# Kernel tuning notes

Hardware: AMD Instinct MI355X
Metric: run time of the kernel (lower is better)

## Reference

```python
import jax, jax.numpy as jnp
import numpy as np

SEQ = 512; WIN = [4, 4, 4]; INNER = 5; DM = 256; H = 4; DK = 64; NEG = -1e9

def _all_sizes():
    s = [SEQ]
    for w in WIN:
        s.append(s[-1] // w)
    return s

def _build_mask():
    # Pyraformer get_mask: intra-scale band (inner_size) + inter-scale parent/child links.
    sizes = _all_sizes(); N = sum(sizes)
    starts = np.cumsum([0] + sizes)
    allow = np.zeros((N, N), bool)
    iw = INNER // 2
    for li, sz in enumerate(sizes):
        st = int(starts[li])
        for i in range(st, st + sz):
            allow[i, max(i - iw, st):min(i + iw + 1, st + sz)] = True
    for li in range(1, len(sizes)):
        st = int(starts[li])
        for i in range(st, st + sizes[li]):
            ls = int(starts[li - 1]) + (i - st) * WIN[li - 1]
            rs = st if i == st + sizes[li] - 1 else int(starts[li - 1]) + (i - st + 1) * WIN[li - 1]
            allow[i, ls:rs] = True
            allow[ls:rs, i] = True
    return jnp.asarray(~allow)  # True = blocked

def _build_indexes():
    # Pyraformer refer_points: for each base position, index of its node at every scale.
    sizes = _all_sizes(); starts = np.cumsum([0] + sizes)
    idx = np.zeros((SEQ, len(sizes)), np.int32)
    for i in range(SEQ):
        cur = i
        idx[i, 0] = cur
        for j in range(1, len(sizes)):
            inner = cur - int(starts[j - 1])
            cur = int(starts[j]) + min(inner // WIN[j - 1], sizes[j] - 1)
            idx[i, j] = cur
    return jnp.asarray(idx)

def _pos_enc(L, D):
    pos = np.arange(L)[:, None]
    div = np.exp(np.arange(0, D, 2) * (-np.log(10000.0) / D))
    pe = np.zeros((L, D), np.float32)
    pe[:, 0::2] = np.sin(pos * div)
    pe[:, 1::2] = np.cos(pos * div)
    return jnp.asarray(pe)

MASK = _build_mask()
INDEXES = _build_indexes()
PE = _pos_enc(SEQ, DM)
DN = ('NCH', 'OIH', 'NCH')

def _ln(x, g, b, eps=1e-5):
    m = x.mean(-1, keepdims=True)
    v = ((x - m) ** 2).mean(-1, keepdims=True)
    return (x - m) * jax.lax.rsqrt(v + eps) * g + b

def _forward(x_enc, x_mark, W_val, W_time, b_time, W_down, b_down, W_conv, b_conv, bn_g, bn_b, W_up, b_up, ln_c_g, ln_c_b, Wq, bq, Wk, bk, Wv, bv, Wo, bo, ln1_g, ln1_b, W1f, b1f, W2f, b2f, ln2_g, ln2_b, Wp, bp):
    B = x_enc.shape[0]
    # DataEmbedding: circular k=3 token conv + time-feature linear + fixed positional
    xt = jnp.pad(x_enc.transpose(0, 2, 1), ((0, 0), (0, 0), (1, 1)), mode='wrap')
    val = jax.lax.conv_general_dilated(xt, W_val, (1,), 'VALID', dimension_numbers=DN).transpose(0, 2, 1)
    emb = val + x_mark @ W_time + b_time + PE[None]  # [B, SEQ, DM]
    # CSCM Bottleneck_Construct: down-proj, strided conv pooling per scale, up-proj, concat, LN
    t = (emb @ W_down + b_down).transpose(0, 2, 1)  # [B, 64, SEQ]
    pooled = []
    for i in range(len(WIN)):
        t = jax.lax.conv_general_dilated(t, W_conv[i], (WIN[i],), 'VALID', dimension_numbers=DN) + b_conv[i][None, :, None]
        t = jax.nn.elu(t * bn_g[i][None, :, None] + bn_b[i][None, :, None])
        pooled.append(t)
    pooled = jnp.concatenate(pooled, axis=2).transpose(0, 2, 1) @ W_up + b_up  # [B, 168, DM]
    x = _ln(jnp.concatenate([emb, pooled], axis=1), ln_c_g, ln_c_b)  # [B, 680, DM]
    N = x.shape[1]
    scale = np.float32(1.0 / np.sqrt(DK))
    for l in range(Wq.shape[0]):
        q = (x @ Wq[l] + bq[l]).reshape(B, N, H, DK).transpose(0, 2, 1, 3)
        k = (x @ Wk[l] + bk[l]).reshape(B, N, H, DK).transpose(0, 2, 1, 3)
        v = (x @ Wv[l] + bv[l]).reshape(B, N, H, DK).transpose(0, 2, 1, 3)
        s = jnp.einsum('bhqd,bhkd->bhqk', q, k) * scale
        s = jnp.where(MASK[None, None], NEG, s)
        o = jnp.einsum('bhqk,bhkd->bhqd', jax.nn.softmax(s, axis=-1), v)
        o = o.transpose(0, 2, 1, 3).reshape(B, N, DM) @ Wo[l] + bo[l]
        x = _ln(x + o, ln1_g[l], ln1_b[l])  # post-norm (normalize_before=False)
        f = jax.nn.relu(x @ W1f[l] + b1f[l]) @ W2f[l] + b2f[l]
        x = _ln(x + f, ln2_g[l], ln2_b[l])
    # FC decoder path: gather each position's multi-scale nodes, concat features
    gathered = x[:, INDEXES.reshape(-1)].reshape(B, SEQ, -1)  # [B, SEQ, 4*DM]
    return gathered[:, -1] @ Wp + bp  # [B, 96]

def setup_inputs() -> dict:
    key = jax.random.key(0)
    ks = iter(jax.random.split(key, 64))
    def w(shape, s=0.05):
        return jax.random.normal(next(ks), shape, jnp.float32) * s
    d = {}
    d['x_enc'] = jax.random.normal(next(ks), (32, SEQ, 1), jnp.float32)
    d['x_mark'] = jax.random.normal(next(ks), (32, SEQ, 4), jnp.float32)
    d['W_val'] = w((DM, 1, 3))
    d['W_time'] = w((4, DM)); d['b_time'] = jnp.zeros((DM,), jnp.float32)
    d['W_down'] = w((DM, 64)); d['b_down'] = jnp.zeros((64,), jnp.float32)
    d['W_conv'] = w((3, 64, 64, 4)); d['b_conv'] = jnp.zeros((3, 64), jnp.float32)
    d['bn_g'] = jnp.ones((3, 64), jnp.float32); d['bn_b'] = jnp.zeros((3, 64), jnp.float32)
    d['W_up'] = w((64, DM)); d['b_up'] = jnp.zeros((DM,), jnp.float32)
    d['ln_c_g'] = jnp.ones((DM,), jnp.float32); d['ln_c_b'] = jnp.zeros((DM,), jnp.float32)
    d['Wq'] = w((2, DM, DM)); d['bq'] = jnp.zeros((2, DM), jnp.float32)
    d['Wk'] = w((2, DM, DM)); d['bk'] = jnp.zeros((2, DM), jnp.float32)
    d['Wv'] = w((2, DM, DM)); d['bv'] = jnp.zeros((2, DM), jnp.float32)
    d['Wo'] = w((2, DM, DM)); d['bo'] = jnp.zeros((2, DM), jnp.float32)
    d['ln1_g'] = jnp.ones((2, DM), jnp.float32); d['ln1_b'] = jnp.zeros((2, DM), jnp.float32)
    d['W1f'] = w((2, DM, 512)); d['b1f'] = jnp.zeros((2, 512), jnp.float32)
    d['W2f'] = w((2, 512, DM)); d['b2f'] = jnp.zeros((2, DM), jnp.float32)
    d['ln2_g'] = jnp.ones((2, DM), jnp.float32); d['ln2_b'] = jnp.zeros((2, DM), jnp.float32)
    d['Wp'] = w((4 * DM, 96)); d['bp'] = jnp.zeros((96,), jnp.float32)
    return d

def reference(x_enc, x_mark, W_val, W_time, b_time, W_down, b_down, W_conv, b_conv, bn_g, bn_b, W_up, b_up, ln_c_g, ln_c_b, Wq, bq, Wk, bk, Wv, bv, Wo, bo, ln1_g, ln1_b, W1f, b1f, W2f, b2f, ln2_g, ln2_b, Wp, bp):
    return _forward(x_enc, x_mark, W_val, W_time, b_time, W_down, b_down, W_conv, b_conv, bn_g, bn_b, W_up, b_up, ln_c_g, ln_c_b, Wq, bq, Wk, bk, Wv, bv, Wo, bo, ln1_g, ln1_b, W1f, b1f, W2f, b2f, ln2_g, ln2_b, Wp, bp)
```

## Files before the change

kernel.cpp:

```cpp
#include <hip/hip_runtime.h>
#include <hip/hip_bf16.h>
#include <math.h>

#define B 32
#define SEQ 512
#define NTOK 680
#define DM 256
#define FF 512
#define NROWS (B*NTOK)

using bf16x8 = __attribute__((ext_vector_type(8))) short;
using f32x4  = __attribute__((ext_vector_type(4))) float;
using u32x4  = __attribute__((ext_vector_type(4))) unsigned int;
typedef __hip_bfloat16 bf16;

__device__ __forceinline__ unsigned short f2bf(float f) {
    union { float f; unsigned u; } x; x.f = f;
    unsigned r = (x.u + 0x7fffu + ((x.u >> 16) & 1u)) >> 16;
    return (unsigned short)r;
}
__device__ __forceinline__ float bfu2f(unsigned short u) {
    union { unsigned u; float f; } x; x.u = ((unsigned)u) << 16;
    return x.f;
}
__device__ __forceinline__ void dotu(unsigned a, unsigned b, float& s) {
    union { unsigned u; float f; } al, ah, bl, bh;
    al.u = a << 16; ah.u = a & 0xffff0000u;
    bl.u = b << 16; bh.u = b & 0xffff0000u;
    s = fmaf(al.f, bl.f, s);
    s = fmaf(ah.f, bh.f, s);
}

__global__ __launch_bounds__(256) void emb_kernel(
    const float* __restrict__ x_enc, const float* __restrict__ x_mark,
    const float* __restrict__ W_val, const float* __restrict__ W_time,
    const float* __restrict__ b_time, float* __restrict__ X, bf16* __restrict__ Xe)
{
    int bs = blockIdx.x;
    int b = bs >> 9, s = bs & 511;
    int d = threadIdx.x;
    int sm1 = (s + 511) & 511, sp1 = (s + 1) & 511;
    float x0 = x_enc[b*512 + sm1];
    float x1 = x_enc[b*512 + s];
    float x2 = x_enc[b*512 + sp1];
    float val = x0 * W_val[d*3+0] + x1 * W_val[d*3+1] + x2 * W_val[d*3+2];
    const float* mk = &x_mark[(size_t)bs*4];
    float tm = mk[0]*W_time[d] + mk[1]*W_time[256+d] + mk[2]*W_time[512+d] + mk[3]*W_time[768+d];
    int i2 = d & ~1;
    float div = expf((float)i2 * (-9.210340371976184f / 256.0f));
    float ang = (float)s * div;
    float pe = (d & 1) ? cosf(ang) : sinf(ang);
    float out = val + tm + b_time[d] + pe;
    X[((size_t)(b*NTOK + s))*DM + d] = out;
    ((unsigned short*)Xe)[(size_t)bs*DM + d] = f2bf(out);
}

__global__ __launch_bounds__(64) void conv_kernel(
    const float* __restrict__ in, int inRPB, int inOff,
    float* __restrict__ Pool, int outOff, int Lout,
    const float* __restrict__ W_conv, const float* __restrict__ b_conv,
    const float* __restrict__ bn_g, const float* __restrict__ bn_b, int sc)
{
    __shared__ float lds[256];
    int blk = blockIdx.x;
    int b = blk / Lout, p = blk % Lout;
    int t = threadIdx.x;
    for (int u = t; u < 256; u += 64)
        lds[u] = in[((size_t)(b*inRPB + inOff + p*4 + (u >> 6)))*64 + (u & 63)];
    __syncthreads();
    float acc = b_conv[sc*64 + t];
    const float* w = &W_conv[(size_t)(sc*64 + t)*256];
    #pragma unroll 4
    for (int ci = 0; ci < 64; ++ci) {
        #pragma unroll
        for (int tap = 0; tap < 4; ++tap)
            acc = fmaf(lds[tap*64 + ci], w[ci*4 + tap], acc);
    }
    float v = acc * bn_g[sc*64 + t] + bn_b[sc*64 + t];
    v = v > 0.f ? v : expm1f(v);
    Pool[((size_t)(b*168 + outOff + p))*64 + t] = v;
}

__global__ __launch_bounds__(256) void up_kernel(
    const float* __restrict__ Pool, const float* __restrict__ W_up,
    const float* __restrict__ b_up, float* __restrict__ X)
{
    __shared__ float row[64];
    int blk = blockIdx.x;
    int b = blk / 168, p = blk % 168;
    int d = threadIdx.x;
    if (d < 64) row[d] = Pool[(size_t)blk*64 + d];
    __syncthreads();
    float acc = b_up[d];
    #pragma unroll 8
    for (int k = 0; k < 64; ++k) acc = fmaf(row[k], W_up[k*256 + d], acc);
    X[((size_t)(b*NTOK + 512 + p))*DM + d] = acc;
}

__global__ __launch_bounds__(256) void ln_kernel(
    const float* __restrict__ Xf, bf16* __restrict__ Xio,
    const float* __restrict__ g, const float* __restrict__ bta)
{
    int r = blockIdx.x*4 + (threadIdx.x >> 6);
    int lane = threadIdx.x & 63;
    float4 v = ((const float4*)(Xf + (size_t)r*DM))[lane];
    float s = v.x + v.y + v.z + v.w;
    #pragma unroll
    for (int o = 32; o; o >>= 1) s += __shfl_xor(s, o);
    float mean = s * (1.0f/256.0f);
    float dx = v.x-mean, dy = v.y-mean, dz = v.z-mean, dw = v.w-mean;
    float q = dx*dx + dy*dy + dz*dz + dw*dw;
    #pragma unroll
    for (int o = 32; o; o >>= 1) q += __shfl_xor(q, o);
    float inv = rsqrtf(q*(1.0f/256.0f) + 1e-5f);
    float4 gg = ((const float4*)g)[lane];
    float4 bb = ((const float4*)bta)[lane];
    float ox = dx*inv*gg.x + bb.x;
    float oy = dy*inv*gg.y + bb.y;
    float oz = dz*inv*gg.z + bb.z;
    float ow = dw*inv*gg.w + bb.w;
    unsigned u0 = (unsigned)f2bf(ox) | ((unsigned)f2bf(oy) << 16);
    unsigned u1 = (unsigned)f2bf(oz) | ((unsigned)f2bf(ow) << 16);
    ((uint2*)(Xio + (size_t)r*DM))[lane] = make_uint2(u0, u1);
}

__global__ void nbr_kernel(int* __restrict__ nbr, int* __restrict__ ncnt)
{
    int i = blockIdx.x * 64 + threadIdx.x;
    if (i >= NTOK) return;
    const int starts[5] = {0, 512, 640, 672, 680};
    int si = (i < 512) ? 0 : (i < 640) ? 1 : (i < 672) ? 2 : 3;
    int st = starts[si], en = starts[si+1];
    int idx = i - st;
    int cnt = 0;
    if (si >= 1) {
        int cs = starts[si-1] + idx*4;
        #pragma unroll
        for (int c = 0; c < 4; ++c) nbr[i*16 + cnt++] = cs + c;
    }
    int lo = (i-2 > st) ? i-2 : st;
    int hi = (i+2 < en-1) ? i+2 : en-1;
    for (int j = lo; j <= hi; ++j) nbr[i*16 + cnt++] = j;
    if (si <= 2) nbr[i*16 + cnt++] = starts[si+1] + (idx >> 2);
    ncnt[i] = cnt;
}

__global__ __launch_bounds__(256) void attn_kernel(
    const bf16* __restrict__ Q, const bf16* __restrict__ K,
    const bf16* __restrict__ V, bf16* __restrict__ O,
    const int* __restrict__ nbr, const int* __restrict__ ncnt)
{
    __shared__ float wsm[4][16];
    __shared__ int   jsm[4][16];
    int flat = blockIdx.x;
    int row = (flat & 7) * (NROWS/8) + (flat >> 3);
    int n = row % NTOK, b = row / NTOK;
    int h = threadIdx.x >> 6;
    int lane = threadIdx.x & 63;
    int j = lane >> 2, g = lane & 3;
    int cnt = ncnt[n];
    int nj = (j < cnt) ? nbr[n*16 + j] : n;
    int jr = b*NTOK + nj;

    const uint4* qp = (const uint4*)(Q + (size_t)row*DM + h*64 + g*16);
    const uint4* kp = (const uint4*)(K + (size_t)jr*DM + h*64 + g*16);
    uint4 qa = qp[0], qb = qp[1];
    uint4 ka = kp[0], kb = kp[1];
    float s = 0.f;
    dotu(qa.x, ka.x, s); dotu(qa.y, ka.y, s); dotu(qa.z, ka.z, s); dotu(qa.w, ka.w, s);
    dotu(qb.x, kb.x, s); dotu(qb.y, kb.y, s); dotu(qb.z, kb.z, s); dotu(qb.w, kb.w, s);
    s += __shfl_xor(s, 1);
    s += __shfl_xor(s, 2);
    s *= 0.125f;
    if (j >= cnt) s = -1e30f;
    float m = s;
    #pragma unroll
    for (int o = 4; o < 64; o <<= 1) m = fmaxf(m, __shfl_xor(m, o));
    float w = (j < cnt) ? expf(s - m) : 0.f;
    float den = w;
    #pragma unroll
    for (int o = 4; o < 64; o <<= 1) den += __shfl_xor(den, o);
    if (g == 0) { wsm[h][j] = w / den; jsm[h][j] = jr; }
    __syncthreads();

    float acc = 0.f;
    const unsigned short* Vu = (const unsigned short*)V;
    for (int jj = 0; jj < cnt; ++jj) {
        float wv = wsm[h][jj];
        int rr = jsm[h][jj];
        acc = fmaf(wv, bfu2f(Vu[(size_t)rr*DM + h*64 + lane]), acc);
    }
    ((unsigned short*)O)[(size_t)row*DM + h*64 + lane] = f2bf(acc);
}

struct WDesc { const float* src; bf16* dst; int K; int N; };
struct WTable { WDesc d[13]; };
__global__ __launch_bounds__(256) void wconv_kernel(WTable tbl)
{
    __shared__ float lds[32][33];
    WDesc ds = tbl.d[blockIdx.y];
    int ntn = ds.N >> 5;
    int ntiles = (ds.K >> 5) * ntn;
    int tile = blockIdx.x;
    if (tile >= ntiles) return;
    int k0 = (tile / ntn) * 32, n0 = (tile % ntn) * 32;
    int t = threadIdx.x;
    int r = t >> 3, c4 = (t & 7) * 4;
    float4 v = *(const float4*)(ds.src + (size_t)(k0 + r)*ds.N + n0 + c4);
    lds[r][c4+0] = v.x; lds[r][c4+1] = v.y; lds[r][c4+2] = v.z; lds[r][c4+3] = v.w;
    __syncthreads();
    unsigned u0 = (unsigned)f2bf(lds[c4+0][r]) | ((unsigned)f2bf(lds[c4+1][r]) << 16);
    unsigned u1 = (unsigned)f2bf(lds[c4+2][r]) | ((unsigned)f2bf(lds[c4+3][r]) << 16);
    *(uint2*)((unsigned short*)ds.dst + (size_t)(n0 + r)*ds.K + k0 + c4) = make_uint2(u0, u1);
}

#define CSTR 260
__global__ __launch_bounds__(512) void wo_ln_kernel(
    const bf16* __restrict__ Ob, bf16* __restrict__ Xh,
    const bf16* __restrict__ WoT, const float* __restrict__ bo,
    const float* __restrict__ g, const float* __restrict__ bta)
{
    __shared__ __align__(16) char smem[16384 + 33280];
    uint4* AsU = (uint4*)smem;
    const bf16x8* Asv = (const bf16x8*)smem;
    float* ctile = (float*)(smem + 16384);

    int t = threadIdx.x;
    int lane = t & 63, w = t >> 6;
    int nwg = gridDim.x;
    int wg = (blockIdx.x & 7) * (nwg >> 3) + (blockIdx.x >> 3);
    int row0 = wg * 32;
    const unsigned short* Obu = (const unsigned short*)Ob;
    const unsigned short* Xu  = (const unsigned short*)Xh;
    const unsigned short* Wu  = (const unsigned short*)WoT;

    #pragma unroll
    for (int i = 0; i < 2; ++i) {
        int gg = t + i*512, r = gg >> 5, c = gg & 31;
        AsU[r*32 + (c ^ (r & 7))] = *(const uint4*)(Obu + (size_t)(row0 + r)*DM + c*8);
    }

    f32x4 acc[2][2];
    #pragma unroll
    for (int m = 0; m < 2; ++m)
        #pragma unroll
        for (int nn = 0; nn < 2; ++nn)
            #pragma unroll
            for (int q = 0; q < 4; ++q) acc[m][nn][q] = 0.f;
    float bv[2];
    #pragma unroll
    for (int nn = 0; nn < 2; ++nn) bv[nn] = bo[w*32 + nn*16 + (lane & 15)];
    __syncthreads();

    #pragma unroll
    for (int kt = 0; kt < 256; kt += 32) {
        int cg = (kt >> 3) + (lane >> 4);
        bf16x8 af[2];
        #pragma unroll
        for (int m = 0; m < 2; ++m) {
            int ar = m*16 + (lane & 15);
            af[m] = Asv[ar*32 + (cg ^ (ar & 7))];
        }
        #pragma unroll
        for (int nn = 0; nn < 2; ++nn) {
            int nrow = w*32 + nn*16 + (lane & 15);
            bf16x8 bfr = *(const bf16x8*)(Wu + (size_t)nrow*256 + kt + (lane >> 4)*8);
            #pragma unroll
            for (int m = 0; m < 2; ++m)
                acc[m][nn] = __builtin_amdgcn_mfma_f32_16x16x32_bf16(af[m], bfr, acc[m][nn], 0, 0, 0);
        }
    }

    __syncthreads();
    #pragma unroll
    for (int m = 0; m < 2; ++m)
        #pragma unroll
        for (int nn = 0; nn < 2; ++nn) {
            int col = w*32 + nn*16 + (lane & 15);
            #pragma unroll
            for (int q = 0; q < 4; ++q) {
                int row = m*16 + (lane >> 4)*4 + q;
                ctile[row*CSTR + col] = acc[m][nn][q] + bv[nn];
            }
        }
    __syncthreads();
    #pragma unroll
    for (int rr = 0; rr < 4; ++rr) {
        int row = w*4 + rr;
        float4 v = *(const float4*)(ctile + row*CSTR + lane*4);
        uint2 xu = *(const uint2*)(Xu + (size_t)(row0 + row)*DM + lane*4);
        v.x += bfu2f((unsigned short)(xu.x & 0xffffu));
        v.y += bfu2f((unsigned short)(xu.x >> 16));
        v.z += bfu2f((unsigned short)(xu.y & 0xffffu));
        v.w += bfu2f((unsigned short)(xu.y >> 16));
        float s = v.x + v.y + v.z + v.w;
        #pragma unroll
        for (int o = 32; o; o >>= 1) s += __shfl_xor(s, o);
        float mean = s * (1.0f/256.0f);
        float dx = v.x-mean, dy = v.y-mean, dz = v.z-mean, dw = v.w-mean;
        float q2 = dx*dx + dy*dy + dz*dz + dw*dw;
        #pragma unroll
        for (int o = 32; o; o >>= 1) q2 += __shfl_xor(q2, o);
        float inv = rsqrtf(q2*(1.0f/256.0f) + 1e-5f);
        float4 gg = ((const float4*)g)[lane];
        float4 bb = ((const float4*)bta)[lane];
        float ox = dx*inv*gg.x + bb.x;
        float oy = dy*inv*gg.y + bb.y;
        float oz = dz*inv*gg.z + bb.z;
        float ow = dw*inv*gg.w + bb.w;
        unsigned u0 = (unsigned)f2bf(ox) | ((unsigned)f2bf(oy) << 16);
        unsigned u1 = (unsigned)f2bf(oz) | ((unsigned)f2bf(ow) << 16);
        *(uint2*)((unsigned short*)Xh + (size_t)(row0 + row)*DM + lane*4) = make_uint2(u0, u1);
    }
}

#define HSTR 280
__global__ __launch_bounds__(512) void ff_kernel(
    bf16* __restrict__ Xh,
    const bf16* __restrict__ W1t, const float* __restrict__ b1,
    const bf16* __restrict__ W2t, const float* __restrict__ b2,
    const float* __restrict__ g, const float* __restrict__ bta)
{
    __shared__ __align__(16) char smem[16384 + 33280];
    uint4* AsU = (uint4*)smem;
    const bf16x8* Asv = (const bf16x8*)smem;
    unsigned short* hT = (unsigned short*)(smem + 16384);
    float* ctile = (float*)(smem + 16384);

    int t = threadIdx.x;
    int lane = t & 63, w = t >> 6;
    int nwg = gridDim.x;
    int wg = (blockIdx.x & 7) * (nwg >> 3) + (blockIdx.x >> 3);
    int row0 = wg * 32;
    const unsigned short* Xu = (const unsigned short*)Xh;

    #pragma unroll
    for (int i = 0; i < 2; ++i) {
        int gg = t + i*512, r = gg >> 5, c = gg & 31;
        AsU[r*32 + (c ^ (r & 7))] = *(const uint4*)(Xu + (size_t)(row0 + r)*DM + c*8);
    }

    f32x4 acc2[2][2];
    #pragma unroll
    for (int m = 0; m < 2; ++m)
        #pragma unroll
        for (int nn = 0; nn < 2; ++nn)
            #pragma unroll
            for (int q = 0; q < 4; ++q) acc2[m][nn][q] = 0.f;
    float b2v[2];
    #pragma unroll
    for (int nn = 0; nn < 2; ++nn) b2v[nn] = b2[w*32 + nn*16 + (lane & 15)];
    __syncthreads();

    const unsigned short* W1u = (const unsigned short*)W1t;
    const unsigned short* W2u = (const unsigned short*)W2t;

    #pragma unroll
    for (int half = 0; half < 2; ++half) {
        f32x4 acc1[2][2];
        #pragma unroll
        for (int m = 0; m < 2; ++m)
            #pragma unroll
            for (int nn = 0; nn < 2; ++nn)
                #pragma unroll
                for (int q = 0; q < 4; ++q) acc1[m][nn][q] = 0.f;
        #pragma unroll
        for (int kt = 0; kt < 256; kt += 32) {
            int cg = (kt >> 3) + (lane >> 4);
            bf16x8 af[2];
            #pragma unroll
            for (int m = 0; m < 2; ++m) {
                int ar = m*16 + (lane & 15);
                af[m] = Asv[ar*32 + (cg ^ (ar & 7))];
            }
            #pragma unroll
            for (int nn = 0; nn < 2; ++nn) {
                int nrow = half*256 + w*32 + nn*16 + (lane & 15);
                bf16x8 bfr = *(const bf16x8*)(W1u + (size_t)nrow*256 + kt + (lane >> 4)*8);
                #pragma unroll
                for (int m = 0; m < 2; ++m)
                    acc1[m][nn] = __builtin_amdgcn_mfma_f32_16x16x32_bf16(af[m], bfr, acc1[m][nn], 0, 0, 0);
            }
        }
        float b1v[2];
        #pragma unroll
        for (int nn = 0; nn < 2; ++nn) b1v[nn] = b1[half*256 + w*32 + nn*16 + (lane & 15)];
        __syncthreads();
        #pragma unroll
        for (int m = 0; m < 2; ++m)
            #pragma unroll
            for (int nn = 0; nn < 2; ++nn) {
                int col = w*32 + nn*16 + (lane & 15);
                #pragma unroll
                for (int q = 0; q < 4; ++q) {
                    int row = m*16 + (lane >> 4)*4 + q;
                    hT[row*HSTR + col] = f2bf(fmaxf(acc1[m][nn][q] + b1v[nn], 0.f));
                }
            }
        __syncthreads();
        #pragma unroll
        for (int kt = 0; kt < 256; kt += 32) {
            bf16x8 af[2];
            #pragma unroll
            for (int m = 0; m < 2; ++m) {
                int ar = m*16 + (lane & 15);
                af[m] = *(const bf16x8*)(hT + ar*HSTR + kt + (lane >> 4)*8);
            }
            #pragma unroll
            for (int nn = 0; nn < 2; ++nn) {
                int nrow = w*32 + nn*16 + (lane & 15);
                bf16x8 bfr = *(const bf16x8*)(W2u + (size_t)nrow*512 + half*256 + kt + (lane >> 4)*8);
                #pragma unroll
                for (int m = 0; m < 2; ++m)
                    acc2[m][nn] = __builtin_amdgcn_mfma_f32_16x16x32_bf16(af[m], bfr, acc2[m][nn], 0, 0, 0);
            }
        }
    }
    __syncthreads();
    #pragma unroll
    for (int m = 0; m < 2; ++m)
        #pragma unroll
        for (int nn = 0; nn < 2; ++nn) {
            int col = w*32 + nn*16 + (lane & 15);
            #pragma unroll
            for (int q = 0; q < 4; ++q) {
                int row = m*16 + (lane >> 4)*4 + q;
                ctile[row*CSTR + col] = acc2[m][nn][q] + b2v[nn];
            }
        }
    __syncthreads();
    #pragma unroll
    for (int rr = 0; rr < 4; ++rr) {
        int row = w*4 + rr;
        float4 v = *(const float4*)(ctile + row*CSTR + lane*4);
        uint2 xu = *(const uint2*)(Xu + (size_t)(row0 + row)*DM + lane*4);
        v.x += bfu2f((unsigned short)(xu.x & 0xffffu));
        v.y += bfu2f((unsigned short)(xu.x >> 16));
        v.z += bfu2f((unsigned short)(xu.y & 0xffffu));
        v.w += bfu2f((unsigned short)(xu.y >> 16));
        float s = v.x + v.y + v.z + v.w;
        #pragma unroll
        for (int o = 32; o; o >>= 1) s += __shfl_xor(s, o);
        float mean = s * (1.0f/256.0f);
        float dx = v.x-mean, dy = v.y-mean, dz = v.z-mean, dw = v.w-mean;
        float q2 = dx*dx + dy*dy + dz*dz + dw*dw;
        #pragma unroll
        for (int o = 32; o; o >>= 1) q2 += __shfl_xor(q2, o);
        float inv = rsqrtf(q2*(1.0f/256.0f) + 1e-5f);
        float4 gg = ((const float4*)g)[lane];
        float4 bb = ((const float4*)bta)[lane];
        float ox = dx*inv*gg.x + bb.x;
        float oy = dy*inv*gg.y + bb.y;
        float oz = dz*inv*gg.z + bb.z;
        float ow = dw*inv*gg.w + bb.w;
        unsigned u0 = (unsigned)f2bf(ox) | ((unsigned)f2bf(oy) << 16);
        unsigned u1 = (unsigned)f2bf(oz) | ((unsigned)f2bf(ow) << 16);
        *(uint2*)((unsigned short*)Xh + (size_t)(row0 + row)*DM + lane*4) = make_uint2(u0, u1);
    }
}

template<int KD, int NY, int NZ, bool RELU>
__global__ __launch_bounds__(256) void mfma_gemm_fr(
    const bf16* __restrict__ A,
    const bf16* __restrict__ Wt0, const bf16* __restrict__ Wt1, const bf16* __restrict__ Wt2,
    const float* __restrict__ b0, const float* __restrict__ b1, const float* __restrict__ b2,
    bf16* __restrict__ O0, bf16* __restrict__ O1, bf16* __restrict__ O2,
    int Nc, int totalWg)
{
    __shared__ __align__(16) char smem[24576];
    uint4* AsU = (uint4*)smem;
    uint4* BsU = (uint4*)(smem + 8192);
    const bf16x8* Asv = (const bf16x8*)smem;
    const bf16x8* Bsv = (const bf16x8*)(smem + 8192);

    int t = threadIdx.x;
    int lane = t & 63, wid = t >> 6;
    int nwg = gridDim.x;
    int wg = (blockIdx.x & 7) * (nwg >> 3) + (blockIdx.x >> 3);
    if (wg >= totalWg) return;
    int xt = wg / (NY*NZ);
    int rem = wg % (NY*NZ);
    int z = rem / NY;
    int y = rem % NY;
    int row0 = xt * 64;
    int n0 = y * 128;
    const bf16* W = ((z == 0) ? Wt0 : (z == 1) ? Wt1 : Wt2) + (size_t)n0*KD;
    const float* bias = (z == 0) ? b0 : (z == 1) ? b1 : b2;
    bf16* Op = (z == 0) ? O0 : (z == 1) ? O1 : O2;

    f32x4 acc[4][2];
    #pragma unroll
    for (int i = 0; i < 4; ++i)
        #pragma unroll
        for (int jn = 0; jn < 2; ++jn)
            #pragma unroll
            for (int r = 0; r < 4; ++r) acc[i][jn][r] = 0.f;

    uint4 pa[2], pb[4];
    #pragma unroll
    for (int i = 0; i < 2; ++i) {
        int gg = t + i*256, r = gg >> 3, c = gg & 7;
        pa[i] = *reinterpret_cast<const uint4*>(A + (size_t)(row0 + r)*KD + c*8);
    }
    #pragma unroll
    for (int i = 0; i < 4; ++i) {
        int gg = t + i*256, r = gg >> 3, c = gg & 7;
        pb[i] = *reinterpret_cast<const uint4*>(W + (size_t)r*KD + c*8);
    }

    #pragma unroll
    for (int kt = 0; kt < KD; kt += 64) {
        __syncthreads();
        #pragma unroll
        for (int i = 0; i < 2; ++i) {
            int gg = t + i*256, r = gg >> 3, c = gg & 7;
            AsU[r*8 + (c ^ (r & 7))] = pa[i];
        }
        #pragma unroll
        for (int i = 0; i < 4; ++i) {
            int gg = t + i*256, r = gg >> 3, c = gg & 7;
            BsU[r*8 + (c ^ (r & 7))] = pb[i];
        }
        __syncthreads();
        if (kt + 64 < KD) {
            #pragma unroll
            for (int i = 0; i < 2; ++i) {
                int gg = t + i*256, r = gg >> 3, c = gg & 7;
                pa[i] = *reinterpret_cast<const uint4*>(A + (size_t)(row0 + r)*KD + (kt + 64) + c*8);
            }
            #pragma unroll
            for (int i = 0; i < 4; ++i) {
                int gg = t + i*256, r = gg >> 3, c = gg & 7;
                pb[i] = *reinterpret_cast<const uint4*>(W + (size_t)r*KD + (kt + 64) + c*8);
            }
        }
        #pragma unroll
        for (int ks = 0; ks < 2; ++ks) {
            int cg = ks*4 + (lane >> 4);
            bf16x8 af[4], bfr[2];
            #pragma unroll
            for (int m = 0; m < 4; ++m) {
                int ar = m*16 + (lane & 15);
                af[m] = Asv[ar*8 + (cg ^ (ar & 7))];
            }
            #pragma unroll
            for (int nn = 0; nn < 2; ++nn) {
                int br = wid*32 + nn*16 + (lane & 15);
                bfr[nn] = Bsv[br*8 + (cg ^ (br & 7))];
            }
            #pragma unroll
            for (int m = 0; m < 4; ++m)
                #pragma unroll
                for (int nn = 0; nn < 2; ++nn)
                    acc[m][nn] = __builtin_amdgcn_mfma_f32_16x16x32_bf16(af[m], bfr[nn], acc[m][nn], 0, 0, 0);
        }
    }

    __syncthreads();
    unsigned short* ctb = (unsigned short*)smem;
    #pragma unroll
    for (int m = 0; m < 4; ++m) {
        #pragma unroll
        for (int nn = 0; nn < 2; ++nn) {
            int cc = wid*32 + nn*16 + (lane & 15);
            float bcol = bias[n0 + cc];
            #pragma unroll
            for (int r = 0; r < 4; ++r) {
                int rr = m*16 + (lane >> 4)*4 + r;
                float v = acc[m][nn][r] + bcol;
                if (RELU) v = fmaxf(v, 0.f);
                ctb[rr*136 + cc] = f2bf(v);
            }
        }
    }
    __syncthreads();
    #pragma unroll
    for (int i = 0; i < 4; ++i) {
        int idx = t + i*256;
        int row = idx >> 4, c8 = (idx & 15) * 8;
        u32x4 uv = *(const u32x4*)(ctb + row*136 + c8);
        *(u32x4*)((unsigned short*)Op + (size_t)(row0 + row)*Nc + n0 + c8) = uv;
    }
}

__global__ __launch_bounds__(256) void mfma_gemm_dn(
    const bf16* __restrict__ A, const bf16* __restrict__ Wt,
    const float* __restrict__ bias, float* __restrict__ Op)
{
    __shared__ __align__(16) char smem[34816];
    uint4* AsU = (uint4*)smem;
    uint4* BsU = (uint4*)(smem + 16384);
    const bf16x8* Asv = (const bf16x8*)smem;
    const bf16x8* Bsv = (const bf16x8*)(smem + 16384);
    const int KD = 256, Nc = 64;

    int t = threadIdx.x;
    int lane = t & 63, wid = t >> 6;
    int wm = wid >> 1, wn = wid & 1;
    int nwg = gridDim.x;
    int wg = (blockIdx.x & 7) * (nwg >> 3) + (blockIdx.x >> 3);
    int row0 = wg * 128;
    int n0 = 0;

    f32x4 acc[4][2];
    #pragma unroll
    for (int i = 0; i < 4; ++i)
        #pragma unroll
        for (int jn = 0; jn < 2; ++jn)
            #pragma unroll
            for (int r = 0; r < 4; ++r) acc[i][jn][r] = 0.f;

    uint4 pa[4], pb[2];
    #pragma unroll
    for (int i = 0; i < 4; ++i) {
        int gg = t + i*256, r = gg >> 3, c = gg & 7;
        pa[i] = *reinterpret_cast<const uint4*>(A + (size_t)(row0 + r)*KD + c*8);
    }
    #pragma unroll
    for (int i = 0; i < 2; ++i) {
        int gg = t + i*256, r = gg >> 3, c = gg & 7;
        pb[i] = *reinterpret_cast<const uint4*>(Wt + (size_t)(n0 + r)*KD + c*8);
    }

    #pragma unroll
    for (int kt = 0; kt < KD; kt += 64) {
        __syncthreads();
        #pragma unroll
        for (int i = 0; i < 4; ++i) {
            int gg = t + i*256, r = gg >> 3, c = gg & 7;
            AsU[r*8 + (c ^ (r & 7))] = pa[i];
        }
        #pragma unroll
        for (int i = 0; i < 2; ++i) {
            int gg = t + i*256, r = gg >> 3, c = gg & 7;
            BsU[r*8 + (c ^ (r & 7))] = pb[i];
        }
        __syncthreads();
        if (kt + 64 < KD) {
            #pragma unroll
            for (int i = 0; i < 4; ++i) {
                int gg = t + i*256, r = gg >> 3, c = gg & 7;
                pa[i] = *reinterpret_cast<const uint4*>(A + (size_t)(row0 + r)*KD + (kt + 64) + c*8);
            }
            #pragma unroll
            for (int i = 0; i < 2; ++i) {
                int gg = t + i*256, r = gg >> 3, c = gg & 7;
                pb[i] = *reinterpret_cast<const uint4*>(Wt + (size_t)(n0 + r)*KD + (kt + 64) + c*8);
            }
        }
        #pragma unroll
        for (int ks = 0; ks < 2; ++ks) {
            int cg = ks*4 + (lane >> 4);
            bf16x8 af[4], bfr[2];
            #pragma unroll
            for (int m = 0; m < 4; ++m) {
                int ar = wm*64 + m*16 + (lane & 15);
                af[m] = Asv[ar*8 + (cg ^ (ar & 7))];
            }
            #pragma unroll
            for (int nn = 0; nn < 2; ++nn) {
                int br = wn*32 + nn*16 + (lane & 15);
                bfr[nn] = Bsv[br*8 + (cg ^ (br & 7))];
            }
            #pragma unroll
            for (int m = 0; m < 4; ++m)
                #pragma unroll
                for (int nn = 0; nn < 2; ++nn)
                    acc[m][nn] = __builtin_amdgcn_mfma_f32_16x16x32_bf16(af[m], bfr[nn], acc[m][nn], 0, 0, 0);
        }
    }

    __syncthreads();
    float* ctile = (float*)smem;
    #pragma unroll
    for (int m = 0; m < 4; ++m) {
        #pragma unroll
        for (int nn = 0; nn < 2; ++nn) {
            int cc = wn*32 + nn*16 + (lane & 15);
            float bcol = bias[n0 + cc];
            #pragma unroll
            for (int r = 0; r < 4; ++r) {
                int rr = wm*64 + m*16 + (lane >> 4)*4 + r;
                ctile[rr*68 + cc] = acc[m][nn][r] + bcol;
            }
        }
    }
    __syncthreads();
    int c4 = (t & 15) * 4;
    #pragma unroll
    for (int rr = t >> 4; rr < 128; rr += 16) {
        float4 v = *reinterpret_cast<const float4*>(ctile + rr*68 + c4);
        *reinterpret_cast<float4*>(Op + (size_t)(row0 + rr)*Nc + n0 + c4) = v;
    }
}

__global__ __launch_bounds__(128) void final_kernel(
    const bf16* __restrict__ Xh, const float* __restrict__ Wp,
    const float* __restrict__ bp, float* __restrict__ out)
{
    __shared__ float rows[1024];
    int b = blockIdx.x, t = threadIdx.x;
    const unsigned short* Xu = (const unsigned short*)Xh;
    for (int u = t; u < 1024; u += 128) {
        int g = u >> 8;
        int id = (g == 0) ? 511 : (g == 1) ? 639 : (g == 2) ? 671 : 679;
        rows[u] = bfu2f(Xu[((size_t)(b*NTOK + id))*DM + (u & 255)]);
    }
    __syncthreads();
    if (t < 96) {
        float acc = bp[t];
        #pragma unroll 8
        for (int k = 0; k < 1024; ++k) acc = fmaf(rows[k], Wp[k*96 + t], acc);
        out[b*96 + t] = acc;
    }
}

extern "C" void kernel_launch(void* const* d_in, const int* in_sizes, int n_in,
                              void* d_out, int out_size, void* d_ws, size_t ws_size,
                              hipStream_t stream)
{
    const float* x_enc  = (const float*)d_in[0];
    const float* x_mark = (const float*)d_in[1];
    const float* W_val  = (const float*)d_in[2];
    const float* W_time = (const float*)d_in[3];
    const float* b_time = (const float*)d_in[4];
    const float* W_down = (const float*)d_in[5];
    const float* b_down = (const float*)d_in[6];
    const float* W_conv = (const float*)d_in[7];
    const float* b_conv = (const float*)d_in[8];
    const float* bn_g   = (const float*)d_in[9];
    const float* bn_b   = (const float*)d_in[10];
    const float* W_up   = (const float*)d_in[11];
    const float* b_up   = (const float*)d_in[12];
    const float* ln_c_g = (const float*)d_in[13];
    const float* ln_c_b = (const float*)d_in[14];
    const float* Wq     = (const float*)d_in[15];
    const float* bq     = (const float*)d_in[16];
    const float* Wk     = (const float*)d_in[17];
    const float* bk     = (const float*)d_in[18];
    const float* Wv     = (const float*)d_in[19];
    const float* bv     = (const float*)d_in[20];
    const float* Wo     = (const float*)d_in[21];
    const float* bo     = (const float*)d_in[22];
    const float* ln1_g  = (const float*)d_in[23];
    const float* ln1_b  = (const float*)d_in[24];
    const float* W1f    = (const float*)d_in[25];
    const float* b1f    = (const float*)d_in[26];
    const float* W2f    = (const float*)d_in[27];
    const float* b2f    = (const float*)d_in[28];
    const float* ln2_g  = (const float*)d_in[29];
    const float* ln2_b  = (const float*)d_in[30];
    const float* Wp     = (const float*)d_in[31];
    const float* bp     = (const float*)d_in[32];

    const size_t RB = (size_t)NROWS * DM;
    float* ws = (float*)d_ws;
    float* X    = ws;
    float* Td   = X + RB;
    float* Pool = Td + (size_t)B*SEQ*64;
    bf16* bws   = (bf16*)(Pool + (size_t)B*168*64);
    bf16* Xh   = bws;
    bf16* Qh   = Xh  + RB;
    bf16* Kh   = Qh  + RB;
    bf16* Vh   = Kh  + RB;
    bf16* Obh  = Vh  + RB;
    bf16* Xe   = Obh + RB;
    bf16* WqT  = Xe  + (size_t)B*SEQ*DM;
    bf16* WkT  = WqT + 2*65536;
    bf16* WvT  = WkT + 2*65536;
    bf16* WoT  = WvT + 2*65536;
    bf16* W1T  = WoT + 2*65536;
    bf16* W2T  = W1T + 2*131072;
    bf16* WdT  = W2T + 2*131072;
    int*  nbr  = (int*)(WdT + 64*256);
    int*  ncnt = nbr + NTOK*16;

    WTable tbl;
    for (int l = 0; l < 2; ++l) {
        tbl.d[l*6+0] = { Wq  + (size_t)l*65536,  WqT + (size_t)l*65536,  256, 256 };
        tbl.d[l*6+1] = { Wk  + (size_t)l*65536,  WkT + (size_t)l*65536,  256, 256 };
        tbl.d[l*6+2] = { Wv  + (size_t)l*65536,  WvT + (size_t)l*65536,  256, 256 };
        tbl.d[l*6+3] = { Wo  + (size_t)l*65536,  WoT + (size_t)l*65536,  256, 256 };
        tbl.d[l*6+4] = { W1f + (size_t)l*131072, W1T + (size_t)l*131072, 256, 512 };
        tbl.d[l*6+5] = { W2f + (size_t)l*131072, W2T + (size_t)l*131072, 512, 256 };
    }
    tbl.d[12] = { W_down, WdT, 256, 64 };
    wconv_kernel<<<dim3(128, 13), 256, 0, stream>>>(tbl);

    emb_kernel<<<B*SEQ, 256, 0, stream>>>(x_enc, x_mark, W_val, W_time, b_time, X, Xe);
    mfma_gemm_dn<<<128, 256, 0, stream>>>(Xe, WdT, b_down, Td);
    conv_kernel<<<B*128, 64, 0, stream>>>(Td, 512, 0,   Pool, 0,   128, W_conv, b_conv, bn_g, bn_b, 0);
    conv_kernel<<<B*32,  64, 0, stream>>>(Pool, 168, 0,  Pool, 128, 32,  W_conv, b_conv, bn_g, bn_b, 1);
    conv_kernel<<<B*8,   64, 0, stream>>>(Pool, 168, 128,Pool, 160, 8,   W_conv, b_conv, bn_g, bn_b, 2);
    up_kernel<<<B*168, 256, 0, stream>>>(Pool, W_up, b_up, X);
    ln_kernel<<<NROWS/4, 256, 0, stream>>>(X, Xh, ln_c_g, ln_c_b);
    nbr_kernel<<<11, 64, 0, stream>>>(nbr, ncnt);

    const int MT = NROWS/64;
    for (int l = 0; l < 2; ++l) {
        const bf16* wqt = WqT + (size_t)l*65536;
        const bf16* wkt = WkT + (size_t)l*65536;
        const bf16* wvt = WvT + (size_t)l*65536;
        const bf16* wot = WoT + (size_t)l*65536;
        const bf16* w1t = W1T + (size_t)l*131072;
        const bf16* w2t = W2T + (size_t)l*131072;
        const float* bq_ = bq + l*DM; const float* bk_ = bk + l*DM;
        const float* bv_ = bv + l*DM; const float* bo_ = bo + l*DM;
        const float* b1_ = b1f + l*FF; const float* b2_ = b2f + l*DM;

        mfma_gemm_fr<256,2,3,false><<<2048, 256, 0, stream>>>(
            Xh, wqt, wkt, wvt, bq_, bk_, bv_, Qh, Kh, Vh, 256, MT*6);
        attn_kernel<<<NROWS, 256, 0, stream>>>(Qh, Kh, Vh, Obh, nbr, ncnt);
        wo_ln_kernel<<<680, 512, 0, stream>>>(Obh, Xh, wot, bo_, ln1_g + l*DM, ln1_b + l*DM);
        ff_kernel<<<680, 512, 0, stream>>>(Xh, w1t, b1_, w2t, b2_, ln2_g + l*DM, ln2_b + l*DM);
    }

    final_kernel<<<B, 128, 0, stream>>>(Xh, Wp, bp, (float*)d_out);
}
```

Measured before the change: 471.9 us.

## Replace tiled QKV GEMM with row-block kernel reusing X tile across Q/K/V

The generic tiled GEMM, which restaged A and B tiles through LDS for each of Q, K and V, is replaced by a dedicated kernel. Each 512-thread block loads a 32-row X tile into LDS once and reuses it for all three projections. Weight fragments are read directly from global memory (relying on cache) rather than staged in LDS. This cuts redundant activation loads and launch work, but the weight reads are not staged and use smaller per-wave tiles, which may reduce MFMA efficiency.

```diff
diff --git a/kernel.cpp b/kernel.cpp
--- a/kernel.cpp
+++ b/kernel.cpp
@@ -214,6 +214,90 @@
     *(uint2*)((unsigned short*)ds.dst + (size_t)(n0 + r)*ds.K + k0 + c4) = make_uint2(u0, u1);
 }
 
+__global__ __launch_bounds__(512) void qkv_kernel(
+    const bf16* __restrict__ Xh,
+    const bf16* __restrict__ WqT, const bf16* __restrict__ WkT, const bf16* __restrict__ WvT,
+    const float* __restrict__ bq, const float* __restrict__ bk, const float* __restrict__ bv,
+    bf16* __restrict__ Qh, bf16* __restrict__ Kh, bf16* __restrict__ Vh)
+{
+    __shared__ __align__(16) char smem[16384 + 16896];
+    uint4* AsU = (uint4*)smem;
+    const bf16x8* Asv = (const bf16x8*)smem;
+    unsigned short* ctb = (unsigned short*)(smem + 16384);
+
+    int t = threadIdx.x;
+    int lane = t & 63, w = t >> 6;
+    int nwg = gridDim.x;
+    int wg = (blockIdx.x & 7) * (nwg >> 3) + (blockIdx.x >> 3);
+    int row0 = wg * 32;
+    const unsigned short* Xu = (const unsigned short*)Xh;
+
+    #pragma unroll
+    for (int i = 0; i < 2; ++i) {
+        int gg = t + i*512, r = gg >> 5, c = gg & 31;
+        AsU[r*32 + (c ^ (r & 7))] = *(const uint4*)(Xu + (size_t)(row0 + r)*DM + c*8);
+    }
+    __syncthreads();
+
+    #pragma unroll
+    for (int z = 0; z < 3; ++z) {
+        const unsigned short* Wu = (const unsigned short*)((z == 0) ? WqT : (z == 1) ? WkT : WvT);
+        const float* bias = (z == 0) ? bq : (z == 1) ? bk : bv;
+        bf16* Op = (z == 0) ? Qh : (z == 1) ? Kh : Vh;
+
+        f32x4 acc[2][2];
+        #pragma unroll
+        for (int m = 0; m < 2; ++m)
+            #pragma unroll
+            for (int nn = 0; nn < 2; ++nn)
+                #pragma unroll
+                for (int q = 0; q < 4; ++q) acc[m][nn][q] = 0.f;
+        float bv_[2];
+        #pragma unroll
+        for (int nn = 0; nn < 2; ++nn) bv_[nn] = bias[w*32 + nn*16 + (lane & 15)];
+
+        #pragma unroll
+        for (int kt = 0; kt < 256; kt += 32) {
+            int cg = (kt >> 3) + (lane >> 4);
+            bf16x8 af[2];
+            #pragma unroll
+            for (int m = 0; m < 2; ++m) {
+                int ar = m*16 + (lane & 15);
+                af[m] = Asv[ar*32 + (cg ^ (ar & 7))];
+            }
+            #pragma unroll
+            for (int nn = 0; nn < 2; ++nn) {
+                int nrow = w*32 + nn*16 + (lane & 15);
+                bf16x8 bfr = *(const bf16x8*)(Wu + (size_t)nrow*256 + kt + (lane >> 4)*8);
+                #pragma unroll
+                for (int m = 0; m < 2; ++m)
+                    acc[m][nn] = __builtin_amdgcn_mfma_f32_16x16x32_bf16(af[m], bfr, acc[m][nn], 0, 0, 0);
+            }
+        }
+
+        __syncthreads();
+        #pragma unroll
+        for (int m = 0; m < 2; ++m)
+            #pragma unroll
+            for (int nn = 0; nn < 2; ++nn) {
+                int col = w*32 + nn*16 + (lane & 15);
+                #pragma unroll
+                for (int q = 0; q < 4; ++q) {
+                    int row = m*16 + (lane >> 4)*4 + q;
+                    ctb[row*264 + col] = f2bf(acc[m][nn][q] + bv_[nn]);
+                }
+            }
+        __syncthreads();
+        #pragma unroll
+        for (int i = 0; i < 2; ++i) {
+            int idx = t + i*512;
+            int row = idx >> 5, c16 = idx & 31;
+            u32x4 uv = *(const u32x4*)(ctb + row*264 + c16*8);
+            *(u32x4*)((unsigned short*)Op + (size_t)(row0 + row)*DM + c16*8) = uv;
+        }
+    }
+}
+
 #define CSTR 260
 __global__ __launch_bounds__(512) void wo_ln_kernel(
     const bf16* __restrict__ Ob, bf16* __restrict__ Xh,
@@ -456,130 +540,6 @@
         unsigned u0 = (unsigned)f2bf(ox) | ((unsigned)f2bf(oy) << 16);
         unsigned u1 = (unsigned)f2bf(oz) | ((unsigned)f2bf(ow) << 16);
         *(uint2*)((unsigned short*)Xh + (size_t)(row0 + row)*DM + lane*4) = make_uint2(u0, u1);
-    }
-}
-
-template<int KD, int NY, int NZ, bool RELU>
-__global__ __launch_bounds__(256) void mfma_gemm_fr(
-    const bf16* __restrict__ A,
-    const bf16* __restrict__ Wt0, const bf16* __restrict__ Wt1, const bf16* __restrict__ Wt2,
-    const float* __restrict__ b0, const float* __restrict__ b1, const float* __restrict__ b2,
-    bf16* __restrict__ O0, bf16* __restrict__ O1, bf16* __restrict__ O2,
-    int Nc, int totalWg)
-{
-    __shared__ __align__(16) char smem[24576];
-    uint4* AsU = (uint4*)smem;
-    uint4* BsU = (uint4*)(smem + 8192);
-    const bf16x8* Asv = (const bf16x8*)smem;
-    const bf16x8* Bsv = (const bf16x8*)(smem + 8192);
-
-    int t = threadIdx.x;
-    int lane = t & 63, wid = t >> 6;
-    int nwg = gridDim.x;
-    int wg = (blockIdx.x & 7) * (nwg >> 3) + (blockIdx.x >> 3);
-    if (wg >= totalWg) return;
-    int xt = wg / (NY*NZ);
-    int rem = wg % (NY*NZ);
-    int z = rem / NY;
-    int y = rem % NY;
-    int row0 = xt * 64;
-    int n0 = y * 128;
-    const bf16* W = ((z == 0) ? Wt0 : (z == 1) ? Wt1 : Wt2) + (size_t)n0*KD;
-    const float* bias = (z == 0) ? b0 : (z == 1) ? b1 : b2;
-    bf16* Op = (z == 0) ? O0 : (z == 1) ? O1 : O2;
-
-    f32x4 acc[4][2];
-    #pragma unroll
-    for (int i = 0; i < 4; ++i)
-        #pragma unroll
-        for (int jn = 0; jn < 2; ++jn)
-            #pragma unroll
-            for (int r = 0; r < 4; ++r) acc[i][jn][r] = 0.f;
-
-    uint4 pa[2], pb[4];
-    #pragma unroll
-    for (int i = 0; i < 2; ++i) {
-        int gg = t + i*256, r = gg >> 3, c = gg & 7;
-        pa[i] = *reinterpret_cast<const uint4*>(A + (size_t)(row0 + r)*KD + c*8);
-    }
-    #pragma unroll
-    for (int i = 0; i < 4; ++i) {
-        int gg = t + i*256, r = gg >> 3, c = gg & 7;
-        pb[i] = *reinterpret_cast<const uint4*>(W + (size_t)r*KD + c*8);
-    }
-
-    #pragma unroll
-    for (int kt = 0; kt < KD; kt += 64) {
-        __syncthreads();
-        #pragma unroll
-        for (int i = 0; i < 2; ++i) {
-            int gg = t + i*256, r = gg >> 3, c = gg & 7;
-            AsU[r*8 + (c ^ (r & 7))] = pa[i];
-        }
-        #pragma unroll
-        for (int i = 0; i < 4; ++i) {
-            int gg = t + i*256, r = gg >> 3, c = gg & 7;
-            BsU[r*8 + (c ^ (r & 7))] = pb[i];
-        }
-        __syncthreads();
-        if (kt + 64 < KD) {
-            #pragma unroll
-            for (int i = 0; i < 2; ++i) {
-                int gg = t + i*256, r = gg >> 3, c = gg & 7;
-                pa[i] = *reinterpret_cast<const uint4*>(A + (size_t)(row0 + r)*KD + (kt + 64) + c*8);
-            }
-            #pragma unroll
-            for (int i = 0; i < 4; ++i) {
-                int gg = t + i*256, r = gg >> 3, c = gg & 7;
-                pb[i] = *reinterpret_cast<const uint4*>(W + (size_t)r*KD + (kt + 64) + c*8);
-            }
-        }
-        #pragma unroll
-        for (int ks = 0; ks < 2; ++ks) {
-            int cg = ks*4 + (lane >> 4);
-            bf16x8 af[4], bfr[2];
-            #pragma unroll
-            for (int m = 0; m < 4; ++m) {
-                int ar = m*16 + (lane & 15);
-                af[m] = Asv[ar*8 + (cg ^ (ar & 7))];
-            }
-            #pragma unroll
-            for (int nn = 0; nn < 2; ++nn) {
-                int br = wid*32 + nn*16 + (lane & 15);
-                bfr[nn] = Bsv[br*8 + (cg ^ (br & 7))];
-            }
-            #pragma unroll
-            for (int m = 0; m < 4; ++m)
-                #pragma unroll
-                for (int nn = 0; nn < 2; ++nn)
-                    acc[m][nn] = __builtin_amdgcn_mfma_f32_16x16x32_bf16(af[m], bfr[nn], acc[m][nn], 0, 0, 0);
-        }
-    }
-
-    __syncthreads();
-    unsigned short* ctb = (unsigned short*)smem;
-    #pragma unroll
-    for (int m = 0; m < 4; ++m) {
-        #pragma unroll
-        for (int nn = 0; nn < 2; ++nn) {
-            int cc = wid*32 + nn*16 + (lane & 15);
-            float bcol = bias[n0 + cc];
-            #pragma unroll
-            for (int r = 0; r < 4; ++r) {
-                int rr = m*16 + (lane >> 4)*4 + r;
-                float v = acc[m][nn][r] + bcol;
-                if (RELU) v = fmaxf(v, 0.f);
-                ctb[rr*136 + cc] = f2bf(v);
-            }
-        }
-    }
-    __syncthreads();
-    #pragma unroll
-    for (int i = 0; i < 4; ++i) {
-        int idx = t + i*256;
-        int row = idx >> 4, c8 = (idx & 15) * 8;
-        u32x4 uv = *(const u32x4*)(ctb + row*136 + c8);
-        *(u32x4*)((unsigned short*)Op + (size_t)(row0 + row)*Nc + n0 + c8) = uv;
     }
 }
 
@@ -796,7 +756,6 @@
     ln_kernel<<<NROWS/4, 256, 0, stream>>>(X, Xh, ln_c_g, ln_c_b);
     nbr_kernel<<<11, 64, 0, stream>>>(nbr, ncnt);
 
-    const int MT = NROWS/64;
     for (int l = 0; l < 2; ++l) {
         const bf16* wqt = WqT + (size_t)l*65536;
         const bf16* wkt = WkT + (size_t)l*65536;
@@ -808,8 +767,7 @@
         const float* bv_ = bv + l*DM; const float* bo_ = bo + l*DM;
         const float* b1_ = b1f + l*FF; const float* b2_ = b2f + l*DM;
 
-        mfma_gemm_fr<256,2,3,false><<<2048, 256, 0, stream>>>(
-            Xh, wqt, wkt, wvt, bq_, bk_, bv_, Qh, Kh, Vh, 256, MT*6);
+        qkv_kernel<<<680, 512, 0, stream>>>(Xh, wqt, wkt, wvt, bq_, bk_, bv_, Qh, Kh, Vh);
         attn_kernel<<<NROWS, 256, 0, stream>>>(Qh, Kh, Vh, Obh, nbr, ncnt);
         wo_ln_kernel<<<680, 512, 0, stream>>>(Obh, Xh, wot, bo_, ln1_g + l*DM, ln1_b + l*DM);
         ff_kernel<<<680, 512, 0, stream>>>(Xh, w1t, b1_, w2t, b2_, ln2_g + l*DM, ln2_b + l*DM);
```

Result: faster. 422.6 us (-10.4%).
